# Kernel optimization log

Measured on AMD Instinct MI355X. Metric: run time of the kernel, lower is better.

Reference implementation:

```python
import math
import jax, jax.numpy as jnp
import numpy as np

HIDDEN = 2048
HEAD_DIM = 128
NUM_HEADS = 32
NUM_KV_HEADS = 8
GROUP = NUM_HEADS // NUM_KV_HEADS
B, S = 1, 2048


def setup_inputs() -> dict:
    key = jax.random.key(0)
    ks = jax.random.split(key, 9)
    scale_in = 1.0 / math.sqrt(HIDDEN)
    scale_o = 1.0 / math.sqrt(NUM_HEADS * HEAD_DIM)
    x = jax.random.normal(ks[0], (B, S, HIDDEN), dtype=jnp.float32)
    # causal mask (1,1,S,S), int32; masked positions are 0
    mask = jnp.tril(jnp.ones((S, S), dtype=jnp.int32))[None, None]
    wq = jax.random.uniform(ks[1], (HIDDEN, NUM_HEADS * HEAD_DIM), jnp.float32, -scale_in, scale_in)
    bq = jax.random.uniform(ks[2], (NUM_HEADS * HEAD_DIM,), jnp.float32, -scale_in, scale_in)
    wk = jax.random.uniform(ks[3], (HIDDEN, NUM_KV_HEADS * HEAD_DIM), jnp.float32, -scale_in, scale_in)
    bk = jax.random.uniform(ks[4], (NUM_KV_HEADS * HEAD_DIM,), jnp.float32, -scale_in, scale_in)
    wv = jax.random.uniform(ks[5], (HIDDEN, NUM_KV_HEADS * HEAD_DIM), jnp.float32, -scale_in, scale_in)
    bv = jax.random.uniform(ks[6], (NUM_KV_HEADS * HEAD_DIM,), jnp.float32, -scale_in, scale_in)
    wo = jax.random.uniform(ks[7], (NUM_HEADS * HEAD_DIM, HIDDEN), jnp.float32, -scale_o, scale_o)
    bo = jax.random.uniform(ks[8], (HIDDEN,), jnp.float32, -scale_o, scale_o)
    return {"x": x, "mask": mask, "wq": wq, "bq": bq, "wk": wk, "bk": bk,
            "wv": wv, "bv": bv, "wo": wo, "bo": bo}


def reference(x, mask, wq, bq, wk, bk, wv, bv, wo, bo):
    Bb, Ss, _ = x.shape
    inv_sqrt_d = 1.0 / math.sqrt(HEAD_DIM)
    # projections
    q = (x @ wq + bq).reshape(Bb, Ss, NUM_KV_HEADS, GROUP, HEAD_DIM)  # grouped query heads
    k = (x @ wk + bk).reshape(Bb, Ss, NUM_KV_HEADS, HEAD_DIM)
    v = (x @ wv + bv).reshape(Bb, Ss, NUM_KV_HEADS, HEAD_DIM)
    # repeat_interleave(group, dim=2) on k/v == broadcasting each kv head over its
    # GROUP consecutive query heads; einsum avoids the physical KV blow-up.
    scores = jnp.einsum('bqhgd,bshd->bhgqs', q, k) * inv_sqrt_d  # (B, Hkv, G, S, S)
    m = mask[:, :, None]  # (1,1,1,S,S) broadcasts over (Hkv, G)
    scores = jnp.where(m == 0, -jnp.inf, scores)
    attn = jax.nn.softmax(scores, axis=-1)
    out = jnp.einsum('bhgqs,bshd->bqhgd', attn, v).reshape(Bb, Ss, NUM_HEADS * HEAD_DIM)
    return out @ wo + bo
```

## Files before the change

kernel.cpp:

```cpp
#include <hip/hip_runtime.h>

#define HIDDEN 2048
#define S_LEN  2048
#define NH     32
#define NKV    8
#define HD     128
#define QKVN   6144
#define OD     4096

typedef float  f32x4   __attribute__((ext_vector_type(4)));
typedef float  f32x16  __attribute__((ext_vector_type(16)));
typedef __bf16 bf16x8  __attribute__((ext_vector_type(8)));
typedef __bf16 bf16x4  __attribute__((ext_vector_type(4)));
typedef unsigned int u32;

static __device__ __forceinline__ f32x4 mfma16(bf16x8 a, bf16x8 b, f32x4 c) {
  return __builtin_amdgcn_mfma_f32_16x16x32_bf16(a, b, c, 0, 0, 0);
}
static __device__ __forceinline__ f32x16 mfma32(bf16x8 a, bf16x8 b, f32x16 c) {
  return __builtin_amdgcn_mfma_f32_32x32x16_bf16(a, b, c, 0, 0, 0);
}
static __device__ __forceinline__ void gload_lds16(const void* g, void* l) {
  __builtin_amdgcn_global_load_lds(
      (__attribute__((address_space(1))) void*)(g),
      (__attribute__((address_space(3))) void*)(l), 16, 0, 0);
}
static __device__ __forceinline__ u32 pk_bf16(float lo, float hi) {
  u32 r;
  asm("v_cvt_pk_bf16_f32 %0, %1, %2" : "=v"(r) : "v"(lo), "v"(hi));
  return r;
}

__global__ __launch_bounds__(256) void k_cvt(const float* __restrict__ in,
                                             __bf16* __restrict__ out, int n) {
  int i = (blockIdx.x * 256 + threadIdx.x) * 4;
  if (i >= n) return;
  float4 v = *reinterpret_cast<const float4*>(in + i);
  bf16x4 o = {(__bf16)v.x, (__bf16)v.y, (__bf16)v.z, (__bf16)v.w};
  *reinterpret_cast<bf16x4*>(out + i) = o;
}

__global__ __launch_bounds__(256) void k_transpose_cvt(const float* __restrict__ src,
                                                       __bf16* __restrict__ dst,
                                                       int K, int N) {
  __shared__ float tile[32][33];
  int tx = threadIdx.x & 31, ty = threadIdx.x >> 5;
  int n0 = blockIdx.x * 32, k0 = blockIdx.y * 32;
#pragma unroll
  for (int r = 0; r < 4; r++) {
    int k = ty + r * 8;
    tile[k][tx] = src[(size_t)(k0 + k) * N + n0 + tx];
  }
  __syncthreads();
#pragma unroll
  for (int r = 0; r < 4; r++) {
    int n = ty + r * 8;
    dst[(size_t)(n0 + n) * K + k0 + tx] = (__bf16)tile[tx][n];
  }
}

__global__ void k_bias_concat(const float* __restrict__ bq, const float* __restrict__ bk,
                              const float* __restrict__ bv, float* __restrict__ out) {
  int i = blockIdx.x * 256 + threadIdx.x;
  if (i >= QKVN) return;
  out[i] = (i < 4096) ? bq[i] : (i < 5120 ? bk[i - 4096] : bv[i - 5120]);
}

__global__ __launch_bounds__(256) void k_vtrans(const __bf16* __restrict__ qkv,
                                                __bf16* __restrict__ vt) {
  __shared__ __bf16 tile[32][33];
  int tx = threadIdx.x & 31, ty = threadIdx.x >> 5;
  int s0 = blockIdx.x * 32, d0 = blockIdx.y * 32, kv = blockIdx.z;
#pragma unroll
  for (int r = 0; r < 4; r++) {
    int s = ty + r * 8;
    tile[s][tx] = qkv[(size_t)(s0 + s) * QKVN + 5120 + kv * HD + d0 + tx];
  }
  __syncthreads();
#pragma unroll
  for (int r = 0; r < 4; r++) {
    int d = ty + r * 8;
    vt[(size_t)(kv * HD + d0 + d) * S_LEN + s0 + tx] = tile[tx][d];
  }
}

template <typename OutT>
__global__ __launch_bounds__(256) void k_gemm_bt(const __bf16* __restrict__ A,
                                                 const __bf16* __restrict__ BT,
                                                 const float* __restrict__ bias,
                                                 OutT* __restrict__ C, int M, int N, int K,
                                                 float oscale, int scale_cols) {
  __shared__ __bf16 Al[128 * 64];
  __shared__ __bf16 Bl[128 * 64];
  const int tid = threadIdx.x;
  const int lane = tid & 63;
  const int w = tid >> 6;
  const int m0 = blockIdx.y * 128;
  const int n0 = blockIdx.x * 128;
  const int wm = (w >> 1) * 64;
  const int wn = (w & 1) * 64;
  const int l15 = lane & 15, lhi = lane >> 4;

  f32x4 acc[4][4];
#pragma unroll
  for (int i = 0; i < 4; i++)
#pragma unroll
    for (int j = 0; j < 4; j++)
#pragma unroll
      for (int e = 0; e < 4; e++) acc[i][j][e] = 0.f;

  for (int kt = 0; kt < K; kt += 64) {
#pragma unroll
    for (int it = 0; it < 4; it++) {
      int idx = it * 256 + tid;
      int row = idx >> 3, slot = idx & 7;
      int scol = ((slot * 16) ^ ((row & 7) << 4)) >> 1;
      gload_lds16(A + (size_t)(m0 + row) * K + kt + scol, &Al[idx * 8]);
      gload_lds16(BT + (size_t)(n0 + row) * K + kt + scol, &Bl[idx * 8]);
    }
    __syncthreads();
#pragma unroll
    for (int kk = 0; kk < 2; kk++) {
      bf16x8 af[4], bfr[4];
#pragma unroll
      for (int i = 0; i < 4; i++) {
        int ra = wm + i * 16 + l15;
        int ba = (kk * 64 + lhi * 16) ^ ((ra & 7) << 4);
        af[i] = *(const bf16x8*)((const char*)Al + ra * 128 + ba);
        int rb = wn + i * 16 + l15;
        int bb = (kk * 64 + lhi * 16) ^ ((rb & 7) << 4);
        bfr[i] = *(const bf16x8*)((const char*)Bl + rb * 128 + bb);
      }
#pragma unroll
      for (int i = 0; i < 4; i++)
#pragma unroll
        for (int j = 0; j < 4; j++) acc[i][j] = mfma16(af[i], bfr[j], acc[i][j]);
    }
    __syncthreads();
  }
#pragma unroll
  for (int j = 0; j < 4; j++) {
    int col = n0 + wn + j * 16 + l15;
    float bv = bias[col];
    float sc = (col < scale_cols) ? oscale : 1.0f;
#pragma unroll
    for (int i = 0; i < 4; i++) {
      int r0 = m0 + wm + i * 16 + lhi * 4;
#pragma unroll
      for (int rr = 0; rr < 4; rr++) {
        C[(size_t)(r0 + rr) * N + col] = (OutT)((acc[i][j][rr] + bv) * sc);
      }
    }
  }
}

__global__ __launch_bounds__(256) void k_gemm_part(const __bf16* __restrict__ A,
                                                   const __bf16* __restrict__ BT,
                                                   float* __restrict__ Cpart,
                                                   int M, int N, int K, int KC) {
  __shared__ __bf16 Al[128 * 64];
  __shared__ __bf16 Bl[128 * 64];
  const int tid = threadIdx.x;
  const int lane = tid & 63;
  const int w = tid >> 6;
  const int m0 = blockIdx.y * 128;
  const int n0 = blockIdx.x * 128;
  const int kbeg = blockIdx.z * KC;
  const int wm = (w >> 1) * 64;
  const int wn = (w & 1) * 64;
  const int l15 = lane & 15, lhi = lane >> 4;

  f32x4 acc[4][4];
#pragma unroll
  for (int i = 0; i < 4; i++)
#pragma unroll
    for (int j = 0; j < 4; j++)
#pragma unroll
      for (int e = 0; e < 4; e++) acc[i][j][e] = 0.f;

  for (int kt = kbeg; kt < kbeg + KC; kt += 64) {
#pragma unroll
    for (int it = 0; it < 4; it++) {
      int idx = it * 256 + tid;
      int row = idx >> 3, slot = idx & 7;
      int scol = ((slot * 16) ^ ((row & 7) << 4)) >> 1;
      gload_lds16(A + (size_t)(m0 + row) * K + kt + scol, &Al[idx * 8]);
      gload_lds16(BT + (size_t)(n0 + row) * K + kt + scol, &Bl[idx * 8]);
    }
    __syncthreads();
#pragma unroll
    for (int kk = 0; kk < 2; kk++) {
      bf16x8 af[4], bfr[4];
#pragma unroll
      for (int i = 0; i < 4; i++) {
        int ra = wm + i * 16 + l15;
        int ba = (kk * 64 + lhi * 16) ^ ((ra & 7) << 4);
        af[i] = *(const bf16x8*)((const char*)Al + ra * 128 + ba);
        int rb = wn + i * 16 + l15;
        int bb = (kk * 64 + lhi * 16) ^ ((rb & 7) << 4);
        bfr[i] = *(const bf16x8*)((const char*)Bl + rb * 128 + bb);
      }
#pragma unroll
      for (int i = 0; i < 4; i++)
#pragma unroll
        for (int j = 0; j < 4; j++) acc[i][j] = mfma16(af[i], bfr[j], acc[i][j]);
    }
    __syncthreads();
  }
  float* C = Cpart + (size_t)blockIdx.z * M * N;
#pragma unroll
  for (int j = 0; j < 4; j++) {
    int col = n0 + wn + j * 16 + l15;
#pragma unroll
    for (int i = 0; i < 4; i++) {
      int r0 = m0 + wm + i * 16 + lhi * 4;
#pragma unroll
      for (int rr = 0; rr < 4; rr++) {
        C[(size_t)(r0 + rr) * N + col] = acc[i][j][rr];
      }
    }
  }
}

__global__ __launch_bounds__(256) void k_ocombine(const float* __restrict__ a,
                                                  const float* __restrict__ b,
                                                  const float* __restrict__ bias,
                                                  float* __restrict__ out) {
  int i = (blockIdx.x * 256 + threadIdx.x) * 4;
  f32x4 va = *(const f32x4*)(a + i);
  f32x4 vb = *(const f32x4*)(b + i);
  f32x4 vbias = *(const f32x4*)(bias + (i & (HIDDEN - 1)));
  f32x4 r = va + vb + vbias;
  *(f32x4*)(out + i) = r;
}

__global__ __launch_bounds__(256, 2) void k_attn(const __bf16* __restrict__ qkv,
                                                 const __bf16* __restrict__ vt,
                                                 __bf16* __restrict__ o) {
  __shared__ __bf16 Kl[2][8192];
  __shared__ __bf16 Vl[2][8192];
  const int tid = threadIdx.x, lane = tid & 63, w = tid >> 6;
  const int l31 = lane & 31, h = lane >> 5;

  const int id = blockIdx.x;
  int tile, head;
  if (id < 256) { head = id >> 4; tile = id & 15; }
  else          { head = 16 + ((id - 256) >> 4); tile = 15 - (id & 15); }
  const int kvh = head >> 2;
  const int qbase = tile * 128 + w * 32;
  const int qg = qbase + l31;
  const int kdiag = (qbase + 31) >> 6;
  const int nkt = 2 * tile + 2;

  bf16x8 qf[8];
  {
    const __bf16* qrow = qkv + (size_t)qg * QKVN + head * HD;
#pragma unroll
    for (int dk = 0; dk < 8; dk++) qf[dk] = *(const bf16x8*)(qrow + dk * 16 + h * 8);
  }

  f32x16 acc[4];
#pragma unroll
  for (int dt = 0; dt < 4; dt++)
#pragma unroll
    for (int r = 0; r < 16; r++) acc[dt][r] = 0.f;
  float m = -INFINITY, lsum = 0.f;

#define STAGE(buf, ktile)                                                           \
  do {                                                                              \
    const int kk0 = (ktile) * 64;                                                   \
    _Pragma("unroll") for (int it = 0; it < 4; it++) {                              \
      int c = it * 256 + tid;                                                       \
      int key = c >> 4, slot = c & 15;                                              \
      int scol = ((slot * 16) ^ ((key & 15) << 4)) >> 1;                            \
      gload_lds16(qkv + (size_t)(kk0 + key) * QKVN + 4096 + kvh * HD + scol,        \
                  &Kl[buf][c * 8]);                                                 \
    }                                                                               \
    _Pragma("unroll") for (int it = 0; it < 4; it++) {                              \
      int c = it * 256 + tid;                                                       \
      int d = c >> 3, slot = c & 7;                                                 \
      int scol = ((slot * 16) ^ ((d & 7) << 4)) >> 1;                               \
      gload_lds16(vt + (size_t)(kvh * HD + d) * S_LEN + kk0 + scol,                 \
                  &Vl[buf][c * 8]);                                                 \
    }                                                                               \
  } while (0)

  STAGE(0, 0);
  __syncthreads();

  for (int kt = 0; kt < nkt; kt++) {
    const int cur = kt & 1;
    if (kt + 1 < nkt) STAGE(cur ^ 1, kt + 1);

    if (kt <= kdiag) {
      const char* Kb = (const char*)&Kl[cur][0];
      const char* Vb = (const char*)&Vl[cur][0];
      const int k0 = kt * 64;
      f32x16 sacc[2];
#pragma unroll
      for (int b = 0; b < 2; b++)
#pragma unroll
        for (int r = 0; r < 16; r++) sacc[b][r] = 0.f;
      __builtin_amdgcn_s_setprio(1);
#pragma unroll
      for (int dk = 0; dk < 8; dk++) {
        const int sA = ((2 * dk + h) ^ (l31 & 15)) * 16;
        bf16x8 kf0 = *(const bf16x8*)(Kb + l31 * 256 + sA);
        bf16x8 kf1 = *(const bf16x8*)(Kb + (32 + l31) * 256 + sA);
        sacc[0] = mfma32(kf0, qf[dk], sacc[0]);
        sacc[1] = mfma32(kf1, qf[dk], sacc[1]);
      }
      __builtin_amdgcn_s_setprio(0);
      float p[32];
#pragma unroll
      for (int b = 0; b < 2; b++)
#pragma unroll
        for (int r = 0; r < 16; r++) p[b * 16 + r] = sacc[b][r];
      if (kt == kdiag) {
#pragma unroll
        for (int b = 0; b < 2; b++)
#pragma unroll
          for (int r = 0; r < 16; r++) {
            int keyg = k0 + b * 32 + (r & 3) + 8 * (r >> 2) + 4 * h;
            if (keyg > qg) p[b * 16 + r] = -INFINITY;
          }
      }
      float t16[16], t8[8], t4[4];
#pragma unroll
      for (int i = 0; i < 16; i++) t16[i] = fmaxf(p[2 * i], p[2 * i + 1]);
#pragma unroll
      for (int i = 0; i < 8; i++) t8[i] = fmaxf(t16[2 * i], t16[2 * i + 1]);
#pragma unroll
      for (int i = 0; i < 4; i++) t4[i] = fmaxf(t8[2 * i], t8[2 * i + 1]);
      float pm = fmaxf(fmaxf(t4[0], t4[1]), fmaxf(t4[2], t4[3]));
      pm = fmaxf(pm, __shfl_xor(pm, 32));
      if (__any(pm - m > 8.f)) {
        float mn = fmaxf(m, pm);
        float corr = __expf(m - mn);
        m = mn;
        lsum *= corr;
#pragma unroll
        for (int dt = 0; dt < 4; dt++)
#pragma unroll
          for (int r = 0; r < 16; r++) acc[dt][r] *= corr;
      }
      float psum = 0.f;
#pragma unroll
      for (int i = 0; i < 32; i++) { p[i] = __expf(p[i] - m); psum += p[i]; }
      lsum += psum;
#pragma unroll
      for (int ks2 = 0; ks2 < 4; ks2++) {
        const int o8 = (ks2 >> 1) * 16 + (ks2 & 1) * 8;
        u32 W0 = pk_bf16(p[o8 + 0], p[o8 + 1]);
        u32 W1 = pk_bf16(p[o8 + 2], p[o8 + 3]);
        u32 W2 = pk_bf16(p[o8 + 4], p[o8 + 5]);
        u32 W3 = pk_bf16(p[o8 + 6], p[o8 + 7]);
        asm("v_permlane32_swap_b32 %0, %1" : "+v"(W0), "+v"(W2));
        asm("v_permlane32_swap_b32 %0, %1" : "+v"(W1), "+v"(W3));
        union { u32 wd[4]; bf16x8 v; } pu;
        pu.wd[0] = W0; pu.wd[1] = W1; pu.wd[2] = W2; pu.wd[3] = W3;
        __builtin_amdgcn_s_setprio(1);
#pragma unroll
        for (int dt = 0; dt < 4; dt++) {
          const int dr = dt * 32 + l31;
          const int sV = ((2 * ks2 + h) ^ (dr & 7)) * 16;
          bf16x8 vf = *(const bf16x8*)(Vb + dr * 128 + sV);
          acc[dt] = mfma32(vf, pu.v, acc[dt]);
        }
        __builtin_amdgcn_s_setprio(0);
      }
    }
    __syncthreads();
  }
#undef STAGE

  lsum += __shfl_xor(lsum, 32);
  const float inv = 1.f / lsum;
  __bf16* orow = o + (size_t)qg * OD + head * HD;
#pragma unroll
  for (int dt = 0; dt < 4; dt++)
#pragma unroll
    for (int rq = 0; rq < 4; rq++) {
      int d = dt * 32 + 8 * rq + 4 * h;
      bf16x4 ov = {(__bf16)(acc[dt][rq * 4 + 0] * inv), (__bf16)(acc[dt][rq * 4 + 1] * inv),
                   (__bf16)(acc[dt][rq * 4 + 2] * inv), (__bf16)(acc[dt][rq * 4 + 3] * inv)};
      *(bf16x4*)(orow + d) = ov;
    }
}

extern "C" void kernel_launch(void* const* d_in, const int* in_sizes, int n_in,
                              void* d_out, int out_size, void* d_ws, size_t ws_size,
                              hipStream_t stream) {
  const float* x  = (const float*)d_in[0];
  const float* wq = (const float*)d_in[2];
  const float* bq = (const float*)d_in[3];
  const float* wk = (const float*)d_in[4];
  const float* bk = (const float*)d_in[5];
  const float* wv = (const float*)d_in[6];
  const float* bv = (const float*)d_in[7];
  const float* wo = (const float*)d_in[8];
  const float* bo = (const float*)d_in[9];
  float* out = (float*)d_out;

  const size_t MB = 1024 * 1024;
  char* ws = (char*)d_ws;
  __bf16* xb    = (__bf16*)(ws);
  __bf16* wqkvT = (__bf16*)(ws + 8 * MB);
  __bf16* woT   = (__bf16*)(ws + 32 * MB);
  __bf16* qkvb  = (__bf16*)(ws + 48 * MB);
  __bf16* vtb   = (__bf16*)(ws + 72 * MB);
  __bf16* ob    = (__bf16*)(ws + 76 * MB);
  float*  bqkv  = (float*)(ws + 92 * MB);
  float*  Cpart = (float*)(ws);

  k_cvt<<<4096, 256, 0, stream>>>(x, xb, HIDDEN * S_LEN);
  k_transpose_cvt<<<dim3(128, 64), 256, 0, stream>>>(wq, wqkvT, HIDDEN, 4096);
  k_transpose_cvt<<<dim3(32, 64), 256, 0, stream>>>(wk, wqkvT + (size_t)4096 * HIDDEN, HIDDEN, 1024);
  k_transpose_cvt<<<dim3(32, 64), 256, 0, stream>>>(wv, wqkvT + (size_t)5120 * HIDDEN, HIDDEN, 1024);
  k_transpose_cvt<<<dim3(64, 128), 256, 0, stream>>>(wo, woT, 4096, HIDDEN);
  k_bias_concat<<<24, 256, 0, stream>>>(bq, bk, bv, bqkv);

  k_gemm_bt<__bf16><<<dim3(QKVN / 128, S_LEN / 128), 256, 0, stream>>>(
      xb, wqkvT, bqkv, qkvb, S_LEN, QKVN, HIDDEN, 0.08838834764831845f, 4096);
  k_vtrans<<<dim3(S_LEN / 32, HD / 32, NKV), 256, 0, stream>>>(qkvb, vtb);
  k_attn<<<512, 256, 0, stream>>>(qkvb, vtb, ob);
  k_gemm_part<<<dim3(HIDDEN / 128, S_LEN / 128, 2), 256, 0, stream>>>(
      ob, woT, Cpart, S_LEN, HIDDEN, OD, OD / 2);
  k_ocombine<<<(S_LEN * HIDDEN) / 1024, 256, 0, stream>>>(
      Cpart, Cpart + (size_t)S_LEN * HIDDEN, bo, out);
}
```

Baseline: 236.5 us.

## Replace QKV projection GEMM with 256x256 double-buffered 8-wave pipelined kernel

Swaps the 128x128 single-buffered QKV GEMM for a 256x256-tile kernel using 512 threads, with LDS double buffering split into k-halves. Global-to-LDS prefetch of the next tile is interleaved with MFMA phases under explicit waitcnt and barrier scheduling, and MFMA priority is raised. The goal is to hide load latency and cut LDS and global traffic per FLOP. The cost is a larger LDS footprint, more registers, and only 192 blocks, which may underfill the 256 CUs.

```diff
diff --git a/kernel.cpp b/kernel.cpp
--- a/kernel.cpp
+++ b/kernel.cpp
@@ -84,71 +84,137 @@
   }
 }
 
-template <typename OutT>
-__global__ __launch_bounds__(256) void k_gemm_bt(const __bf16* __restrict__ A,
-                                                 const __bf16* __restrict__ BT,
-                                                 const float* __restrict__ bias,
-                                                 OutT* __restrict__ C, int M, int N, int K,
-                                                 float oscale, int scale_cols) {
-  __shared__ __bf16 Al[128 * 64];
-  __shared__ __bf16 Bl[128 * 64];
-  const int tid = threadIdx.x;
-  const int lane = tid & 63;
-  const int w = tid >> 6;
-  const int m0 = blockIdx.y * 128;
-  const int n0 = blockIdx.x * 128;
-  const int wm = (w >> 1) * 64;
-  const int wn = (w & 1) * 64;
+__global__ __launch_bounds__(512, 2) void k_gemm8(const __bf16* __restrict__ A,
+                                                  const __bf16* __restrict__ BT,
+                                                  const float* __restrict__ bias,
+                                                  __bf16* __restrict__ C,
+                                                  int M, int N, int K,
+                                                  float oscale, int scale_cols) {
+  __shared__ __bf16 Al[2][2][8192];
+  __shared__ __bf16 Bl[2][2][8192];
+  const int tid = threadIdx.x, lane = tid & 63, w = tid >> 6;
   const int l15 = lane & 15, lhi = lane >> 4;
-
-  f32x4 acc[4][4];
-#pragma unroll
-  for (int i = 0; i < 4; i++)
+  const int wr = w >> 2, wc = w & 3;
+  const int mt = blockIdx.x & 7, nt = blockIdx.x >> 3;
+  const int m0 = mt * 256, n0 = nt * 256;
+  const int NKT = K >> 6;
+  const __bf16* Ab = A + (size_t)m0 * K;
+  const __bf16* Bb = BT + (size_t)n0 * K;
+
+  f32x4 acc[8][4];
+#pragma unroll
+  for (int i = 0; i < 8; i++)
 #pragma unroll
     for (int j = 0; j < 4; j++)
 #pragma unroll
       for (int e = 0; e < 4; e++) acc[i][j][e] = 0.f;
 
-  for (int kt = 0; kt < K; kt += 64) {
-#pragma unroll
-    for (int it = 0; it < 4; it++) {
-      int idx = it * 256 + tid;
-      int row = idx >> 3, slot = idx & 7;
-      int scol = ((slot * 16) ^ ((row & 7) << 4)) >> 1;
-      gload_lds16(A + (size_t)(m0 + row) * K + kt + scol, &Al[idx * 8]);
-      gload_lds16(BT + (size_t)(n0 + row) * K + kt + scol, &Bl[idx * 8]);
-    }
-    __syncthreads();
-#pragma unroll
-    for (int kk = 0; kk < 2; kk++) {
-      bf16x8 af[4], bfr[4];
-#pragma unroll
-      for (int i = 0; i < 4; i++) {
-        int ra = wm + i * 16 + l15;
-        int ba = (kk * 64 + lhi * 16) ^ ((ra & 7) << 4);
-        af[i] = *(const bf16x8*)((const char*)Al + ra * 128 + ba);
-        int rb = wn + i * 16 + l15;
-        int bb = (kk * 64 + lhi * 16) ^ ((rb & 7) << 4);
-        bfr[i] = *(const bf16x8*)((const char*)Bl + rb * 128 + bb);
-      }
-#pragma unroll
-      for (int i = 0; i < 4; i++)
-#pragma unroll
-        for (int j = 0; j < 4; j++) acc[i][j] = mfma16(af[i], bfr[j], acc[i][j]);
-    }
-    __syncthreads();
-  }
+#define SGH(dstA, srcB, buf, kh, ktile)                                           \
+  do {                                                                            \
+    _Pragma("unroll") for (int it = 0; it < 2; ++it) {                            \
+      int c = it * 512 + tid;                                                     \
+      int row = c >> 2, slot = c & 3;                                             \
+      int scol = ((slot * 16) ^ (((row >> 1) & 3) << 4)) >> 1;                    \
+      gload_lds16(srcB + (size_t)row * K + (ktile) * 64 + (kh) * 32 + scol,       \
+                  &dstA[buf][kh][c * 8]);                                         \
+    }                                                                             \
+  } while (0)
+
+#define RD_A(cb, kk)                                                              \
+  do {                                                                            \
+    _Pragma("unroll") for (int i = 0; i < 8; ++i) {                               \
+      int row = wr * 128 + i * 16 + l15;                                          \
+      af[i] = *(const bf16x8*)(&Al[cb][kk][row * 32 +                             \
+                (((lhi * 16) ^ (((row >> 1) & 3) << 4)) >> 1)]);                  \
+    }                                                                             \
+  } while (0)
+
+#define RD_B(cb, kk, nh)                                                          \
+  do {                                                                            \
+    _Pragma("unroll") for (int j = 0; j < 2; ++j) {                               \
+      int row = wc * 64 + (nh) * 32 + j * 16 + l15;                               \
+      bfr[j] = *(const bf16x8*)(&Bl[cb][kk][row * 32 +                            \
+                (((lhi * 16) ^ (((row >> 1) & 3) << 4)) >> 1)]);                  \
+    }                                                                             \
+  } while (0)
+
+#define MFMA_PH(nh)                                                               \
+  do {                                                                            \
+    __builtin_amdgcn_s_setprio(1);                                                \
+    _Pragma("unroll") for (int i = 0; i < 8; ++i) {                               \
+      acc[i][2 * (nh)] = mfma16(af[i], bfr[0], acc[i][2 * (nh)]);                 \
+      acc[i][2 * (nh) + 1] = mfma16(af[i], bfr[1], acc[i][2 * (nh) + 1]);         \
+    }                                                                             \
+    __builtin_amdgcn_s_setprio(0);                                                \
+  } while (0)
+
+  SGH(Al, Ab, 0, 0, 0);
+  SGH(Bl, Bb, 0, 0, 0);
+  SGH(Al, Ab, 0, 1, 0);
+  SGH(Bl, Bb, 0, 1, 0);
+  asm volatile("s_waitcnt vmcnt(4)" ::: "memory");
+  __builtin_amdgcn_s_barrier();
+  __builtin_amdgcn_sched_barrier(0);
+
+  for (int kt = 0; kt < NKT; ++kt) {
+    const int cb = kt & 1, pb = cb ^ 1;
+    const bool pf = (kt + 1 < NKT);
+    bf16x8 af[8], bfr[2];
+
+    RD_A(cb, 0);
+    RD_B(cb, 0, 0);
+    if (pf) SGH(Al, Ab, pb, 0, kt + 1);
+    __builtin_amdgcn_s_barrier();
+    asm volatile("s_waitcnt lgkmcnt(0)" ::: "memory");
+    MFMA_PH(0);
+    __builtin_amdgcn_s_barrier();
+    RD_B(cb, 0, 1);
+    if (pf) SGH(Bl, Bb, pb, 0, kt + 1);
+    __builtin_amdgcn_s_barrier();
+    asm volatile("s_waitcnt lgkmcnt(0)" ::: "memory");
+    MFMA_PH(1);
+    if (pf) {
+      asm volatile("s_waitcnt vmcnt(4)" ::: "memory");
+    } else {
+      asm volatile("s_waitcnt vmcnt(0)" ::: "memory");
+    }
+    __builtin_amdgcn_s_barrier();
+    __builtin_amdgcn_sched_barrier(0);
+
+    RD_A(cb, 1);
+    RD_B(cb, 1, 0);
+    if (pf) SGH(Al, Ab, pb, 1, kt + 1);
+    __builtin_amdgcn_s_barrier();
+    asm volatile("s_waitcnt lgkmcnt(0)" ::: "memory");
+    MFMA_PH(0);
+    __builtin_amdgcn_s_barrier();
+    RD_B(cb, 1, 1);
+    if (pf) SGH(Bl, Bb, pb, 1, kt + 1);
+    __builtin_amdgcn_s_barrier();
+    asm volatile("s_waitcnt lgkmcnt(0)" ::: "memory");
+    MFMA_PH(1);
+    if (pf) {
+      asm volatile("s_waitcnt vmcnt(4)" ::: "memory");
+    }
+    __builtin_amdgcn_s_barrier();
+    __builtin_amdgcn_sched_barrier(0);
+  }
+#undef SGH
+#undef RD_A
+#undef RD_B
+#undef MFMA_PH
+
 #pragma unroll
   for (int j = 0; j < 4; j++) {
-    int col = n0 + wn + j * 16 + l15;
+    int col = n0 + wc * 64 + j * 16 + l15;
     float bv = bias[col];
     float sc = (col < scale_cols) ? oscale : 1.0f;
 #pragma unroll
-    for (int i = 0; i < 4; i++) {
-      int r0 = m0 + wm + i * 16 + lhi * 4;
+    for (int i = 0; i < 8; i++) {
+      int r0 = m0 + wr * 128 + i * 16 + lhi * 4;
 #pragma unroll
       for (int rr = 0; rr < 4; rr++) {
-        C[(size_t)(r0 + rr) * N + col] = (OutT)((acc[i][j][rr] + bv) * sc);
+        C[(size_t)(r0 + rr) * N + col] = (__bf16)((acc[i][j][rr] + bv) * sc);
       }
     }
   }
@@ -420,8 +486,8 @@
   k_transpose_cvt<<<dim3(64, 128), 256, 0, stream>>>(wo, woT, 4096, HIDDEN);
   k_bias_concat<<<24, 256, 0, stream>>>(bq, bk, bv, bqkv);
 
-  k_gemm_bt<__bf16><<<dim3(QKVN / 128, S_LEN / 128), 256, 0, stream>>>(
-      xb, wqkvT, bqkv, qkvb, S_LEN, QKVN, HIDDEN, 0.08838834764831845f, 4096);
+  k_gemm8<<<192, 512, 0, stream>>>(xb, wqkvT, bqkv, qkvb, S_LEN, QKVN, HIDDEN,
+                                   0.08838834764831845f, 4096);
   k_vtrans<<<dim3(S_LEN / 32, HD / 32, NKV), 256, 0, stream>>>(qkvb, vtb);
   k_attn<<<512, 256, 0, stream>>>(qkvb, vtb, ob);
   k_gemm_part<<<dim3(HIDDEN / 128, S_LEN / 128, 2), 256, 0, stream>>>(
```

New measurement: 228.7 us. 3.3% less time.
